# Optimization experiments

Hardware: AMD Instinct MI355X
Metric: run time of the kernel (lower is better)

The kernel has to match this reference:

```python
import jax, jax.numpy as jnp
import numpy as np

EPS = 0.001
NUM_HEAD = 4

def _bn(x, g, b, m, v):
    # x: [B,C,H,W]; per-channel affine batchnorm in eval mode
    inv = g / jnp.sqrt(v + EPS)
    return x * inv[None, :, None, None] + (b - m * inv)[None, :, None, None]

def setup_inputs() -> dict:
    key = jax.random.key(0)
    ks = jax.random.split(key, 16)
    B, C, H, W = 8, 256, 40, 40
    C2 = 2 * C
    return {
        "x": jax.random.normal(ks[0], (B, C, H, W), jnp.float32),
        "qkv_w": jax.random.normal(ks[1], (C2, C), jnp.float32) * 0.05,
        "qkv_g": jax.random.uniform(ks[2], (C2,), jnp.float32),
        "qkv_b": jax.random.normal(ks[3], (C2,), jnp.float32) * 0.05,
        "qkv_m": jax.random.normal(ks[4], (C2,), jnp.float32) * 0.05,
        "qkv_v": jax.random.uniform(ks[5], (C2,), jnp.float32) + 0.5,
        "cb1_w": jax.random.normal(ks[6], (C, 1, 3, 3), jnp.float32) * 0.05,
        "cb1_g": jax.random.uniform(ks[7], (C,), jnp.float32),
        "cb1_b": jax.random.normal(ks[8], (C,), jnp.float32) * 0.05,
        "cb1_m": jax.random.normal(ks[9], (C,), jnp.float32) * 0.05,
        "cb1_v": jax.random.uniform(ks[10], (C,), jnp.float32) + 0.5,
        "cb2_w": jax.random.normal(ks[11], (C, C), jnp.float32) * 0.05,
        "cb2_g": jax.random.uniform(ks[12], (C,), jnp.float32),
        "cb2_b": jax.random.normal(ks[13], (C,), jnp.float32) * 0.05,
        "cb2_m": jax.random.normal(ks[14], (C,), jnp.float32) * 0.05,
        "cb2_v": jax.random.uniform(ks[15], (C,), jnp.float32) + 0.5,
    }

def reference(x, qkv_w, qkv_g, qkv_b, qkv_m, qkv_v,
              cb1_w, cb1_g, cb1_b, cb1_m, cb1_v,
              cb2_w, cb2_g, cb2_b, cb2_m, cb2_v):
    B, C, H, W = x.shape
    nh = NUM_HEAD
    dh = C // nh          # dim_head
    dk = dh // 2          # dim_key
    scale = dk ** -0.5
    L = H * W

    # qkv: 1x1 conv (ch -> 2ch) + BN
    qkv = jnp.einsum('oc,bchw->bohw', qkv_w, x)
    qkv = _bn(qkv, qkv_g, qkv_b, qkv_m, qkv_v)
    qkv = qkv.reshape(B, nh, 2 * dk + dh, L)
    q, k, v = qkv[:, :, :dk], qkv[:, :, dk:2 * dk], qkv[:, :, 2 * dk:]

    # attn = q^T @ k * scale -> softmax over last dim
    attn = jnp.einsum('bndq,bndk->bnqk', q, k) * scale  # [B,nh,L,L]
    attn = jax.nn.softmax(attn, axis=-1)

    # y = v @ attn^T : y[d,q] = sum_k v[d,k] * attn[q,k]
    y = jnp.einsum('bndk,bnqk->bndq', v, attn).reshape(B, C, H, W)

    # depthwise 3x3 conv branch on v + BN
    vr = v.reshape(B, C, H, W)
    dw = jax.lax.conv_general_dilated(
        vr, cb1_w, window_strides=(1, 1), padding=((1, 1), (1, 1)),
        feature_group_count=C, dimension_numbers=('NCHW', 'OIHW', 'NCHW'))
    y = y + _bn(dw, cb1_g, cb1_b, cb1_m, cb1_v)

    # final 1x1 conv + BN
    out = jnp.einsum('oc,bchw->bohw', cb2_w, y)
    return _bn(out, cb2_g, cb2_b, cb2_m, cb2_v)
```

## Files before the change

### kernel.cpp

```cpp
#include <hip/hip_runtime.h>
#include <hip/hip_bf16.h>

#define EPS 1e-3f
#define QSC_LOG2E 0.2550348653f

typedef __attribute__((ext_vector_type(8))) short bf16x8;
typedef __attribute__((ext_vector_type(4))) float f32x4;
typedef __attribute__((ext_vector_type(4))) unsigned short u16x4;
typedef __attribute__((ext_vector_type(8))) unsigned short u16x8;
typedef __attribute__((ext_vector_type(2))) unsigned int u32x2;

typedef const __attribute__((address_space(1))) unsigned int g_u32;
typedef __attribute__((address_space(3))) unsigned int l_u32;

__device__ __forceinline__ unsigned short f2bf(float f) {
    union { float f; unsigned u; } v; v.f = f;
    unsigned r = v.u + 0x7FFFu + ((v.u >> 16) & 1u);
    return (unsigned short)(r >> 16);
}
__device__ __forceinline__ float bf2f(unsigned short h) {
    union { unsigned u; float f; } v; v.u = ((unsigned)h) << 16;
    return v.f;
}
__device__ __forceinline__ unsigned pkbf(float lo, float hi) {
    float2 t; t.x = lo; t.y = hi;
    __hip_bfloat162 h = __float22bfloat162_rn(t);
    union { __hip_bfloat162 h; unsigned u; } c; c.h = h;
    return c.u;
}

__global__ __launch_bounds__(256) void conv_kernel(
    const float* __restrict__ wq, const float* __restrict__ wc,
    unsigned short* __restrict__ wqb, unsigned short* __restrict__ wcb,
    const float* __restrict__ x, unsigned short* __restrict__ xt)
{
    int bid = blockIdx.x;
    int tid = threadIdx.x;
    if (bid < 192) {
        int i = (bid * 256 + tid) * 4;
        const float* src; unsigned short* dst; int off;
        if (i < 131072) { src = wq; dst = wqb; off = i; }
        else            { src = wc; dst = wcb; off = i - 131072; }
        f32x4 v = *(const f32x4*)(src + off);
        u16x4 o;
        #pragma unroll
        for (int j = 0; j < 4; ++j) o[j] = f2bf(v[j]);
        *(u16x4*)(dst + off) = o;
        return;
    }
    __shared__ float t[64][65];
    int bid2 = bid - 192;
    int l0 = (bid2 % 25) * 64, c0 = ((bid2 / 25) & 3) * 64, b = bid2 / 100;
    const float* xb = x + ((size_t)b * 256 + c0) * 1600 + l0;
    #pragma unroll
    for (int p = 0; p < 4; ++p) {
        int row = p * 16 + (tid >> 4);
        int col = (tid & 15) * 4;
        f32x4 v = *(const f32x4*)(xb + (size_t)row * 1600 + col);
        #pragma unroll
        for (int j = 0; j < 4; ++j) t[row][col + j] = v[j];
    }
    __syncthreads();
    int l = tid >> 2, cs = tid & 3;
    u16x8 o0, o1;
    #pragma unroll
    for (int i = 0; i < 8; ++i) o0[i] = f2bf(t[cs * 16 + i][l]);
    #pragma unroll
    for (int i = 0; i < 8; ++i) o1[i] = f2bf(t[cs * 16 + 8 + i][l]);
    unsigned short* dst = xt + ((size_t)b * 1600 + l0 + l) * 256 + c0 + cs * 16;
    *(u16x8*)dst = o0;
    *(u16x8*)(dst + 8) = o1;
}

__global__ __launch_bounds__(256) void qkv_gemm_kernel(
    const unsigned short* __restrict__ wqb, const unsigned short* __restrict__ xt,
    const float* __restrict__ gg, const float* __restrict__ bet,
    const float* __restrict__ mm, const float* __restrict__ vv,
    unsigned short* __restrict__ qk, unsigned short* __restrict__ vt,
    unsigned short* __restrict__ v2)
{
    __shared__ unsigned short ldsT[4][32 * 72];

    const int gl_tile = blockIdx.x % 104;
    const int by = blockIdx.x / 104;
    if (gl_tile >= 100) return;

    const int tid = threadIdx.x, wid = tid >> 6, lane = tid & 63;
    const int g = lane >> 4, cc = lane & 15;
    const int gl0 = gl_tile * 128 + (wid & 1) * 64;
    const int o_base = by * 64 + (wid >> 1) * 32;

    const unsigned short* wb0 = wqb + (size_t)(o_base + cc) * 256;
    const unsigned short* wb1 = wqb + (size_t)(o_base + 16 + cc) * 256;
    const unsigned short* xb  = xt + (size_t)(gl0 + cc) * 256;

    const f32x4 fz = {0.f, 0.f, 0.f, 0.f};
    f32x4 acc[2][4] = {{fz, fz, fz, fz}, {fz, fz, fz, fz}};
    #pragma unroll 4
    for (int kk = 0; kk < 256; kk += 32) {
        bf16x8 a0 = *(const bf16x8*)(wb0 + kk + 8 * g);
        bf16x8 a1 = *(const bf16x8*)(wb1 + kk + 8 * g);
        #pragma unroll
        for (int f = 0; f < 4; ++f) {
            bf16x8 bfr = *(const bf16x8*)(xb + (size_t)f * 16 * 256 + kk + 8 * g);
            acc[0][f] = __builtin_amdgcn_mfma_f32_16x16x32_bf16(a0, bfr, acc[0][f], 0, 0, 0);
            acc[1][f] = __builtin_amdgcn_mfma_f32_16x16x32_bf16(a1, bfr, acc[1][f], 0, 0, 0);
        }
    }

    const int head = by >> 1;
    const bool is_v = by & 1;
    float inv[2][4], bias[2][4];
    #pragma unroll
    for (int i = 0; i < 2; ++i) {
        #pragma unroll
        for (int r = 0; r < 4; ++r) {
            int oc = o_base + 16 * i + 4 * g + r;
            float iv = gg[oc] * rsqrtf(vv[oc] + EPS);
            float bs = bet[oc] - mm[oc] * iv;
            if ((oc & 127) < 32) { iv *= QSC_LOG2E; bs *= QSC_LOG2E; }
            inv[i][r] = iv; bias[i][r] = bs;
        }
    }

    if (!is_v) {
        #pragma unroll
        for (int f = 0; f < 4; ++f) {
            int gl = gl0 + 16 * f + cc;
            int b  = gl / 1600;
            int ll = gl - b * 1600;
            unsigned short* dst = qk + ((size_t)(b * 4 + head) * 1600 + ll) * 64;
            #pragma unroll
            for (int i = 0; i < 2; ++i) {
                u16x4 pk;
                #pragma unroll
                for (int r = 0; r < 4; ++r) pk[r] = f2bf(acc[i][f][r] * inv[i][r] + bias[i][r]);
                *(u16x4*)(dst + (o_base & 63) + 16 * i + 4 * g) = pk;
            }
        }
    } else {
        const int d_base = (o_base & 63);
        #pragma unroll
        for (int f = 0; f < 4; ++f) {
            int gl = gl0 + 16 * f + cc;
            unsigned short* v2dst = v2 + (size_t)gl * 256 + head * 64 + d_base;
            #pragma unroll
            for (int i = 0; i < 2; ++i) {
                u16x4 pk;
                #pragma unroll
                for (int r = 0; r < 4; ++r) {
                    unsigned short h = f2bf(acc[i][f][r] * inv[i][r] + bias[i][r]);
                    pk[r] = h;
                    ldsT[wid][(16 * i + 4 * g + r) * 72 + 16 * f + cc] = h;
                }
                *(u16x4*)(v2dst + 16 * i + 4 * g) = pk;
            }
        }
        asm volatile("s_waitcnt lgkmcnt(0)" ::: "memory");
        #pragma unroll
        for (int j = 0; j < 4; ++j) {
            int p = j * 64 + lane;
            int d_loc = p >> 3, c8 = p & 7;
            u16x8 val = *(const u16x8*)&ldsT[wid][d_loc * 72 + c8 * 8];
            int gl_c = gl0 + c8 * 8;
            int b  = gl_c / 1600;
            int ll = gl_c - b * 1600;
            *(u16x8*)(vt + ((size_t)(b * 4 + head) * 64 + d_base + d_loc) * 1600 + ll) = val;
        }
    }
}

__global__ __launch_bounds__(128) void attn_kernel(
    const unsigned short* __restrict__ qk, const unsigned short* __restrict__ vt,
    unsigned short* __restrict__ pa, unsigned short* __restrict__ pb,
    float* __restrict__ ssum)
{
    __shared__ __align__(16) unsigned short kbuf[2][64 * 32];
    __shared__ __align__(16) unsigned short vbuf[2][64 * 64];

    const int tid = threadIdx.x, wid = tid >> 6, lane = tid & 63;
    const int g = lane >> 4, cc = lane & 15;
    const int combo = blockIdx.x & 63;
    const int pair = combo >> 1;
    const int z = combo & 1;
    const int q0 = (blockIdx.x >> 6) * 64 + wid * 32;

    const int kt_begin = z ? 13 : 0;
    const int NT = z ? 12 : 13;

    const unsigned short* qkb = qk + (size_t)pair * 1600 * 64;
    const unsigned short* vtb = vt + (size_t)pair * 64 * 1600;

    bf16x8 bq0 = *(const bf16x8*)(qkb + (size_t)(q0 + cc) * 64 + 8 * g);
    bf16x8 bq1 = *(const bf16x8*)(qkb + (size_t)(q0 + 16 + cc) * 64 + 8 * g);

    const int krow = tid >> 2, kchk = tid & 3;
    const unsigned short* kP = qkb + (size_t)krow * 64 + 32 + (kchk ^ (krow & 3)) * 8
                              + (size_t)kt_begin * 4096;
    const int vrow = tid >> 3, vchk = tid & 7;
    const unsigned short* vP = vtb + (size_t)vrow * 1600 + (vchk ^ (vrow & 7)) * 8
                              + (size_t)kt_begin * 64;

    const unsigned short* kr0  = &kbuf[0][cc * 32 + (g ^ (cc & 3)) * 8];
    const unsigned short* kr1  = &kbuf[1][cc * 32 + (g ^ (cc & 3)) * 8];
    const unsigned short* vr0a = &vbuf[0][cc * 64 + ((g) ^ (cc & 7)) * 8];
    const unsigned short* vr0b = &vbuf[0][cc * 64 + ((4 + g) ^ (cc & 7)) * 8];
    const unsigned short* vr1a = &vbuf[1][cc * 64 + ((g) ^ (cc & 7)) * 8];
    const unsigned short* vr1b = &vbuf[1][cc * 64 + ((4 + g) ^ (cc & 7)) * 8];

    #define STAGE(bufi)                                                               \
        do {                                                                          \
            __builtin_amdgcn_global_load_lds((g_u32*)kP,                              \
                (l_u32*)(&kbuf[bufi][wid * 512]), 16, 0, 0);                          \
            __builtin_amdgcn_global_load_lds((g_u32*)(kP + 2048),                     \
                (l_u32*)(&kbuf[bufi][1024 + wid * 512]), 16, 0, 0);                   \
            __builtin_amdgcn_global_load_lds((g_u32*)vP,                              \
                (l_u32*)(&vbuf[bufi][wid * 512]), 16, 0, 0);                          \
            __builtin_amdgcn_global_load_lds((g_u32*)(vP + 16 * 1600),                \
                (l_u32*)(&vbuf[bufi][1024 + wid * 512]), 16, 0, 0);                   \
            __builtin_amdgcn_global_load_lds((g_u32*)(vP + 32 * 1600),                \
                (l_u32*)(&vbuf[bufi][2048 + wid * 512]), 16, 0, 0);                   \
            __builtin_amdgcn_global_load_lds((g_u32*)(vP + 48 * 1600),                \
                (l_u32*)(&vbuf[bufi][3072 + wid * 512]), 16, 0, 0);                   \
            kP += 4096; vP += 64;                                                     \
        } while (0)

    const f32x4 fz = {0.f, 0.f, 0.f, 0.f};
    const short one_bf = (short)0x3F80;
    const bf16x8 ones = {one_bf, one_bf, one_bf, one_bf, one_bf, one_bf, one_bf, one_bf};
    f32x4 o[2][4] = {{fz, fz, fz, fz}, {fz, fz, fz, fz}};
    f32x4 sumacc[2] = {fz, fz};

    auto compute = [&](const unsigned short* kr, const unsigned short* vra,
                       const unsigned short* vrb) {
        f32x4 s4[2][4];
        {
            bf16x8 kf[4];
            #pragma unroll
            for (int f = 0; f < 4; ++f)
                kf[f] = *(const bf16x8*)(kr + f * 512);
            __builtin_amdgcn_s_setprio(1);
            #pragma unroll
            for (int f = 0; f < 4; ++f)
                s4[0][f] = __builtin_amdgcn_mfma_f32_16x16x32_bf16(kf[f], bq0, fz, 0, 0, 0);
            #pragma unroll
            for (int f = 0; f < 4; ++f)
                s4[1][f] = __builtin_amdgcn_mfma_f32_16x16x32_bf16(kf[f], bq1, fz, 0, 0, 0);
            __builtin_amdgcn_s_setprio(0);
        }

        unsigned pb_u[2][2][4];
        #pragma unroll
        for (int qf = 0; qf < 2; ++qf) {
            unsigned c2[4][2];
            #pragma unroll
            for (int f = 0; f < 4; ++f) {
                float p0 = exp2f(s4[qf][f][0]), p1 = exp2f(s4[qf][f][1]);
                float p2 = exp2f(s4[qf][f][2]), p3 = exp2f(s4[qf][f][3]);
                c2[f][0] = pkbf(p0, p1);
                c2[f][1] = pkbf(p2, p3);
            }
            #pragma unroll
            for (int s2 = 0; s2 < 2; ++s2) {
                const int fA = 2 * s2, fB = 2 * s2 + 1;
                u32x2 xy0 = __builtin_amdgcn_permlane32_swap(c2[fA][0], c2[fB][0], false, false);
                u32x2 xy1 = __builtin_amdgcn_permlane32_swap(c2[fA][1], c2[fB][1], false, false);
                u32x2 w02 = __builtin_amdgcn_permlane16_swap(xy0.x, xy0.y, false, false);
                u32x2 w13 = __builtin_amdgcn_permlane16_swap(xy1.x, xy1.y, false, false);
                pb_u[qf][s2][0] = w02.x;
                pb_u[qf][s2][1] = w13.x;
                pb_u[qf][s2][2] = w02.y;
                pb_u[qf][s2][3] = w13.y;
            }
        }

        __builtin_amdgcn_s_setprio(1);
        #pragma unroll
        for (int s2 = 0; s2 < 2; ++s2) {
            const unsigned short* vr = s2 ? vrb : vra;
            bf16x8 vf[4];
            #pragma unroll
            for (int f2 = 0; f2 < 4; ++f2)
                vf[f2] = *(const bf16x8*)(vr + f2 * 1024);
            #pragma unroll
            for (int qf = 0; qf < 2; ++qf) {
                union { unsigned u[4]; bf16x8 v; } pbv;
                #pragma unroll
                for (int j = 0; j < 4; ++j) pbv.u[j] = pb_u[qf][s2][j];
                #pragma unroll
                for (int f2 = 0; f2 < 4; ++f2)
                    o[qf][f2] = __builtin_amdgcn_mfma_f32_16x16x32_bf16(vf[f2], pbv.v, o[qf][f2], 0, 0, 0);
                sumacc[qf] = __builtin_amdgcn_mfma_f32_16x16x32_bf16(ones, pbv.v, sumacc[qf], 0, 0, 0);
            }
        }
        __builtin_amdgcn_s_setprio(0);
    };

    STAGE(0);

    for (int t = 0; t + 1 < NT; ++t) {
        STAGE((t + 1) & 1);
        asm volatile("s_waitcnt vmcnt(6)" ::: "memory");
        __builtin_amdgcn_s_barrier();
        if (t & 1) compute(kr1, vr1a, vr1b);
        else       compute(kr0, vr0a, vr0b);
        __builtin_amdgcn_s_barrier();
    }
    asm volatile("s_waitcnt vmcnt(0)" ::: "memory");
    __builtin_amdgcn_s_barrier();
    if ((NT - 1) & 1) compute(kr1, vr1a, vr1b);
    else              compute(kr0, vr0a, vr0b);
    #undef STAGE

    const int n = pair & 3, b = pair >> 2;
    #pragma unroll
    for (int qf = 0; qf < 2; ++qf) {
        unsigned short* pdst = (z ? pb : pa) + ((size_t)b * 1600 + q0 + qf * 16 + cc) * 256 + n * 64;
        #pragma unroll
        for (int f2 = 0; f2 < 4; ++f2) {
            u16x4 st;
            #pragma unroll
            for (int r = 0; r < 4; ++r) st[r] = f2bf(o[qf][f2][r]);
            *(u16x4*)(pdst + 16 * f2 + 4 * g) = st;
        }
    }
    if (lane < 16) {
        ssum[((size_t)z * 32 + b * 4 + n) * 1600 + q0 + cc]      = sumacc[0][0];
        ssum[((size_t)z * 32 + b * 4 + n) * 1600 + q0 + 16 + cc] = sumacc[1][0];
    }
}

__global__ __launch_bounds__(256) void dwout_kernel(
    const unsigned short* __restrict__ v2,
    const unsigned short* __restrict__ pa, const unsigned short* __restrict__ pb,
    const float* __restrict__ ssum,
    const float* __restrict__ cw, const float* __restrict__ g1,
    const float* __restrict__ b1, const float* __restrict__ m1,
    const float* __restrict__ v1,
    const unsigned short* __restrict__ wcb, const float* __restrict__ g2,
    const float* __restrict__ b2, const float* __restrict__ m2,
    const float* __restrict__ vbn2,
    float* __restrict__ out)
{
    __shared__ unsigned short y2s[32][264];

    const int tid = threadIdx.x, wid = tid >> 6, lane = tid & 63;
    const int g = lane >> 4, cc = lane & 15;
    const int gl0 = blockIdx.x * 32;

    {
        const int gl_loc = tid & 31, cpart = tid >> 5;
        const int gl = gl0 + gl_loc;
        const int b = gl / 1600, l = gl - b * 1600;
        const int h = l / 40, w = l - h * 40;
        #pragma unroll
        for (int cg = 0; cg < 4; ++cg) {
            const int c0 = cpart * 32 + cg * 8;
            const int n = c0 >> 6;
            float s0 = ssum[(size_t)(b * 4 + n) * 1600 + l];
            float s1 = ssum[(size_t)(32 + b * 4 + n) * 1600 + l];
            float il = 1.f / (s0 + s1);
            float s[8];
            #pragma unroll
            for (int i = 0; i < 8; ++i) s[i] = 0.f;
            #pragma unroll
            for (int kh = -1; kh <= 1; ++kh) {
                int hh = h + kh;
                if (hh < 0 || hh >= 40) continue;
                #pragma unroll
                for (int kw = -1; kw <= 1; ++kw) {
                    int ww = w + kw;
                    if (ww < 0 || ww >= 40) continue;
                    u16x8 vv8 = *(const u16x8*)(v2 + (size_t)(gl + kh * 40 + kw) * 256 + c0);
                    const int tap = (kh + 1) * 3 + (kw + 1);
                    #pragma unroll
                    for (int i = 0; i < 8; ++i)
                        s[i] = fmaf(bf2f(vv8[i]), cw[(c0 + i) * 9 + tap], s[i]);
                }
            }
            u16x8 ya = *(const u16x8*)(pa + (size_t)gl * 256 + c0);
            u16x8 yb = *(const u16x8*)(pb + (size_t)gl * 256 + c0);
            u16x8 o8;
            #pragma unroll
            for (int i = 0; i < 8; ++i) {
                int c = c0 + i;
                float iv = g1[c] * rsqrtf(v1[c] + EPS);
                float yv = (bf2f(ya[i]) + bf2f(yb[i])) * il;
                o8[i] = f2bf(yv + s[i] * iv + (b1[c] - m1[c] * iv));
            }
            *(u16x8*)&y2s[gl_loc][c0] = o8;
        }
    }
    __syncthreads();

    const int o_base = wid * 64;
    const unsigned short* wb = wcb + (size_t)(o_base + cc) * 256;

    const f32x4 fz = {0.f, 0.f, 0.f, 0.f};
    f32x4 acc[4][2] = {{fz, fz}, {fz, fz}, {fz, fz}, {fz, fz}};
    #pragma unroll 4
    for (int kk = 0; kk < 256; kk += 32) {
        bf16x8 a[4], bfr[2];
        #pragma unroll
        for (int i = 0; i < 4; ++i)
            a[i] = *(const bf16x8*)(wb + (size_t)i * 16 * 256 + kk + 8 * g);
        #pragma unroll
        for (int f = 0; f < 2; ++f)
            bfr[f] = *(const bf16x8*)&y2s[16 * f + cc][kk + 8 * g];
        #pragma unroll
        for (int i = 0; i < 4; ++i)
            #pragma unroll
            for (int f = 0; f < 2; ++f)
                acc[i][f] = __builtin_amdgcn_mfma_f32_16x16x32_bf16(a[i], bfr[f], acc[i][f], 0, 0, 0);
    }
    #pragma unroll
    for (int i = 0; i < 4; ++i) {
        #pragma unroll
        for (int r = 0; r < 4; ++r) {
            int oc = o_base + 16 * i + 4 * g + r;
            float iv = g2[oc] * rsqrtf(vbn2[oc] + EPS);
            float bs = b2[oc] - m2[oc] * iv;
            #pragma unroll
            for (int f = 0; f < 2; ++f) {
                int gl = gl0 + 16 * f + cc;
                int b  = gl / 1600;
                int ll = gl - b * 1600;
                out[((size_t)b * 256 + oc) * 1600 + ll] = acc[i][f][r] * iv + bs;
            }
        }
    }
}

extern "C" void kernel_launch(void* const* d_in, const int* in_sizes, int n_in,
                              void* d_out, int out_size, void* d_ws, size_t ws_size,
                              hipStream_t stream) {
    const float* x     = (const float*)d_in[0];
    const float* qkv_w = (const float*)d_in[1];
    const float* qkv_g = (const float*)d_in[2];
    const float* qkv_b = (const float*)d_in[3];
    const float* qkv_m = (const float*)d_in[4];
    const float* qkv_v = (const float*)d_in[5];
    const float* cb1_w = (const float*)d_in[6];
    const float* cb1_g = (const float*)d_in[7];
    const float* cb1_b = (const float*)d_in[8];
    const float* cb1_m = (const float*)d_in[9];
    const float* cb1_v = (const float*)d_in[10];
    const float* cb2_w = (const float*)d_in[11];
    const float* cb2_g = (const float*)d_in[12];
    const float* cb2_b = (const float*)d_in[13];
    const float* cb2_m = (const float*)d_in[14];
    const float* cb2_v = (const float*)d_in[15];
    float* out = (float*)d_out;

    unsigned short* ws16 = (unsigned short*)d_ws;
    const size_t N16 = 3276800;
    unsigned short* xt  = ws16;
    unsigned short* qk  = ws16 + N16;
    unsigned short* vt  = ws16 + 2 * N16;
    unsigned short* pb_ = ws16 + 3 * N16;
    unsigned short* v2  = ws16 + 4 * N16;
    unsigned short* wqb = ws16 + 5 * N16;
    unsigned short* wcb = wqb + 131072;
    float* ssum = (float*)(wcb + 65536);
    unsigned short* pa = xt;

    conv_kernel<<<dim3(992), 256, 0, stream>>>(qkv_w, cb2_w, wqb, wcb, x, xt);
    qkv_gemm_kernel<<<dim3(832), 256, 0, stream>>>(wqb, xt, qkv_g, qkv_b, qkv_m, qkv_v, qk, vt, v2);
    attn_kernel<<<dim3(1600), 128, 0, stream>>>(qk, vt, pa, pb_, ssum);
    dwout_kernel<<<dim3(400), 256, 0, stream>>>(v2, pa, pb_, ssum,
                                                cb1_w, cb1_g, cb1_b, cb1_m, cb1_v,
                                                wcb, cb2_g, cb2_b, cb2_m, cb2_v, out);
}
```

Baseline: 119.5 us.

## Widen attention blocks to 4 waves covering 128 queries to reuse K/V tiles

Measured after the change: 107.1 us. -10.3%, faster.

```diff
diff --git a/kernel.cpp b/kernel.cpp
--- a/kernel.cpp
+++ b/kernel.cpp
@@ -170,7 +170,7 @@
     }
 }
 
-__global__ __launch_bounds__(128) void attn_kernel(
+__global__ __launch_bounds__(256) void attn_kernel(
     const unsigned short* __restrict__ qk, const unsigned short* __restrict__ vt,
     unsigned short* __restrict__ pa, unsigned short* __restrict__ pb,
     float* __restrict__ ssum)
@@ -183,7 +183,10 @@
     const int combo = blockIdx.x & 63;
     const int pair = combo >> 1;
     const int z = combo & 1;
-    const int q0 = (blockIdx.x >> 6) * 64 + wid * 32;
+    const int qsuper = blockIdx.x >> 6;
+    const int q0 = qsuper * 128 + wid * 16;
+    const bool two = (qsuper < 12);
+    const int q0b = two ? (q0 + 64) : q0;
 
     const int kt_begin = z ? 13 : 0;
     const int NT = z ? 12 : 13;
@@ -192,14 +195,15 @@
     const unsigned short* vtb = vt + (size_t)pair * 64 * 1600;
 
     bf16x8 bq0 = *(const bf16x8*)(qkb + (size_t)(q0 + cc) * 64 + 8 * g);
-    bf16x8 bq1 = *(const bf16x8*)(qkb + (size_t)(q0 + 16 + cc) * 64 + 8 * g);
+    bf16x8 bq1 = *(const bf16x8*)(qkb + (size_t)(q0b + cc) * 64 + 8 * g);
 
     const int krow = tid >> 2, kchk = tid & 3;
     const unsigned short* kP = qkb + (size_t)krow * 64 + 32 + (kchk ^ (krow & 3)) * 8
                               + (size_t)kt_begin * 4096;
     const int vrow = tid >> 3, vchk = tid & 7;
-    const unsigned short* vP = vtb + (size_t)vrow * 1600 + (vchk ^ (vrow & 7)) * 8
+    const unsigned short* vPa = vtb + (size_t)vrow * 1600 + (vchk ^ (vrow & 7)) * 8
                               + (size_t)kt_begin * 64;
+    const unsigned short* vPb = vPa + (size_t)32 * 1600;
 
     const unsigned short* kr0  = &kbuf[0][cc * 32 + (g ^ (cc & 3)) * 8];
     const unsigned short* kr1  = &kbuf[1][cc * 32 + (g ^ (cc & 3)) * 8];
@@ -212,17 +216,11 @@
         do {                                                                          \
             __builtin_amdgcn_global_load_lds((g_u32*)kP,                              \
                 (l_u32*)(&kbuf[bufi][wid * 512]), 16, 0, 0);                          \
-            __builtin_amdgcn_global_load_lds((g_u32*)(kP + 2048),                     \
-                (l_u32*)(&kbuf[bufi][1024 + wid * 512]), 16, 0, 0);                   \
-            __builtin_amdgcn_global_load_lds((g_u32*)vP,                              \
+            __builtin_amdgcn_global_load_lds((g_u32*)vPa,                             \
                 (l_u32*)(&vbuf[bufi][wid * 512]), 16, 0, 0);                          \
-            __builtin_amdgcn_global_load_lds((g_u32*)(vP + 16 * 1600),                \
-                (l_u32*)(&vbuf[bufi][1024 + wid * 512]), 16, 0, 0);                   \
-            __builtin_amdgcn_global_load_lds((g_u32*)(vP + 32 * 1600),                \
+            __builtin_amdgcn_global_load_lds((g_u32*)vPb,                             \
                 (l_u32*)(&vbuf[bufi][2048 + wid * 512]), 16, 0, 0);                   \
-            __builtin_amdgcn_global_load_lds((g_u32*)(vP + 48 * 1600),                \
-                (l_u32*)(&vbuf[bufi][3072 + wid * 512]), 16, 0, 0);                   \
-            kP += 4096; vP += 64;                                                     \
+            kP += 4096; vPa += 64; vPb += 64;                                         \
         } while (0)
 
     const f32x4 fz = {0.f, 0.f, 0.f, 0.f};
@@ -255,8 +253,10 @@
             unsigned c2[4][2];
             #pragma unroll
             for (int f = 0; f < 4; ++f) {
-                float p0 = exp2f(s4[qf][f][0]), p1 = exp2f(s4[qf][f][1]);
-                float p2 = exp2f(s4[qf][f][2]), p3 = exp2f(s4[qf][f][3]);
+                float p0 = __builtin_amdgcn_exp2f(s4[qf][f][0]);
+                float p1 = __builtin_amdgcn_exp2f(s4[qf][f][1]);
+                float p2 = __builtin_amdgcn_exp2f(s4[qf][f][2]);
+                float p3 = __builtin_amdgcn_exp2f(s4[qf][f][3]);
                 c2[f][0] = pkbf(p0, p1);
                 c2[f][1] = pkbf(p2, p3);
             }
@@ -300,7 +300,7 @@
 
     for (int t = 0; t + 1 < NT; ++t) {
         STAGE((t + 1) & 1);
-        asm volatile("s_waitcnt vmcnt(6)" ::: "memory");
+        asm volatile("s_waitcnt vmcnt(3)" ::: "memory");
         __builtin_amdgcn_s_barrier();
         if (t & 1) compute(kr1, vr1a, vr1b);
         else       compute(kr0, vr0a, vr0b);
@@ -313,20 +313,30 @@
     #undef STAGE
 
     const int n = pair & 3, b = pair >> 2;
-    #pragma unroll
-    for (int qf = 0; qf < 2; ++qf) {
-        unsigned short* pdst = (z ? pb : pa) + ((size_t)b * 1600 + q0 + qf * 16 + cc) * 256 + n * 64;
+    {
+        unsigned short* pdst = (z ? pb : pa) + ((size_t)b * 1600 + q0 + cc) * 256 + n * 64;
         #pragma unroll
         for (int f2 = 0; f2 < 4; ++f2) {
             u16x4 st;
             #pragma unroll
-            for (int r = 0; r < 4; ++r) st[r] = f2bf(o[qf][f2][r]);
+            for (int r = 0; r < 4; ++r) st[r] = f2bf(o[0][f2][r]);
             *(u16x4*)(pdst + 16 * f2 + 4 * g) = st;
         }
     }
+    if (two) {
+        unsigned short* pdst = (z ? pb : pa) + ((size_t)b * 1600 + q0b + cc) * 256 + n * 64;
+        #pragma unroll
+        for (int f2 = 0; f2 < 4; ++f2) {
+            u16x4 st;
+            #pragma unroll
+            for (int r = 0; r < 4; ++r) st[r] = f2bf(o[1][f2][r]);
+            *(u16x4*)(pdst + 16 * f2 + 4 * g) = st;
+        }
+    }
     if (lane < 16) {
-        ssum[((size_t)z * 32 + b * 4 + n) * 1600 + q0 + cc]      = sumacc[0][0];
-        ssum[((size_t)z * 32 + b * 4 + n) * 1600 + q0 + 16 + cc] = sumacc[1][0];
+        ssum[((size_t)z * 32 + b * 4 + n) * 1600 + q0 + cc] = sumacc[0][0];
+        if (two)
+            ssum[((size_t)z * 32 + b * 4 + n) * 1600 + q0b + cc] = sumacc[1][0];
     }
 }
 
@@ -466,7 +476,7 @@
 
     conv_kernel<<<dim3(992), 256, 0, stream>>>(qkv_w, cb2_w, wqb, wcb, x, xt);
     qkv_gemm_kernel<<<dim3(832), 256, 0, stream>>>(wqb, xt, qkv_g, qkv_b, qkv_m, qkv_v, qk, vt, v2);
-    attn_kernel<<<dim3(1600), 128, 0, stream>>>(qk, vt, pa, pb_, ssum);
+    attn_kernel<<<dim3(832), 256, 0, stream>>>(qk, vt, pa, pb_, ssum);
     dwout_kernel<<<dim3(400), 256, 0, stream>>>(v2, pa, pb_, ssum,
                                                 cb1_w, cb1_g, cb1_b, cb1_m, cb1_v,
                                                 wcb, cb2_g, cb2_b, cb2_m, cb2_v, out);
```
